# Kernel tuning notes

Hardware: AMD Instinct MI355X
Metric: run time of the kernel (lower is better)

## Reference

```python
import jax, jax.numpy as jnp
import numpy as np

B, D_IN, H, LAT = 4096, 4096, 4096, 512


def setup_inputs() -> dict:
    key = jax.random.key(0)
    ks = jax.random.split(key, 10)
    s = lambda fan_in: 1.0 / np.sqrt(fan_in)
    return {
        "x": jax.random.normal(ks[0], (B, D_IN), jnp.float32),
        "W_e1": jax.random.normal(ks[1], (D_IN, H), jnp.float32) * s(D_IN),
        "b_e1": jax.random.uniform(ks[2], (H,), jnp.float32),
        "W_e2": jax.random.normal(ks[3], (H, 2 * LAT), jnp.float32) * s(H),
        "b_e2": jax.random.uniform(ks[4], (2 * LAT,), jnp.float32),
        "W_d1": jax.random.normal(ks[5], (LAT, H), jnp.float32) * s(LAT),
        "b_d1": jax.random.uniform(ks[6], (H,), jnp.float32),
        "W_d2": jax.random.normal(ks[7], (H, D_IN), jnp.float32) * s(H),
        "b_d2": jax.random.uniform(ks[8], (D_IN,), jnp.float32),
        "eps": jax.random.normal(ks[9], (B, LAT), jnp.float32),
    }


def reference(x, W_e1, b_e1, W_e2, b_e2, W_d1, b_d1, W_d2, b_d2, eps):
    # encoder MLP
    h = jax.nn.relu(x @ W_e1 + b_e1)
    z = h @ W_e2 + b_e2                      # [B, 2*LAT]
    mu, logvar = z[:, :LAT], z[:, LAT:]
    # reparameterize: cholesky(diag(exp(logvar))) @ eps + mu == exp(0.5*logvar)*eps + mu
    zs = mu + jnp.exp(0.5 * logvar) * eps    # [B, LAT]
    # decoder MLP
    hd = jax.nn.relu(zs @ W_d1 + b_d1)
    recon = hd @ W_d2 + b_d2                 # [B, D_IN]
    return recon, mu, logvar
```

## Files before the change

### kernel.cpp

```cpp
#include <hip/hip_runtime.h>
#include <hip/hip_bf16.h>

typedef __attribute__((ext_vector_type(8))) __bf16 bf16x8;
typedef __attribute__((ext_vector_type(4))) float f32x4;
typedef __attribute__((ext_vector_type(4))) unsigned short ushort4v;
typedef unsigned short u16;

__device__ __forceinline__ u16 f2bf_bits(float f) {
    union { float f; unsigned int u; } x; x.f = f;
    unsigned int r = x.u + 0x7FFFu + ((x.u >> 16) & 1u);
    return (u16)(r >> 16);
}

__device__ __forceinline__ void gload_lds16(const void* g, void* l) {
    __builtin_amdgcn_global_load_lds(
        (const __attribute__((address_space(1))) void*)g,
        (__attribute__((address_space(3))) void*)l, 16, 0, 0);
}

#define BARRIER()  __builtin_amdgcn_s_barrier()
#define LGKM0()    asm volatile("s_waitcnt lgkmcnt(0)" ::: "memory")
#define VMW8()     asm volatile("s_waitcnt vmcnt(8)" ::: "memory")
#define VMW0()     asm volatile("s_waitcnt vmcnt(0)" ::: "memory")

__global__ void cvt4(const float* __restrict__ in, u16* __restrict__ out, int n) {
    int i = (blockIdx.x * 256 + threadIdx.x) << 2;
    if (i >= n) return;
    f32x4 v = *reinterpret_cast<const f32x4*>(in + i);
    ushort4v o;
    o.x = f2bf_bits(v.x); o.y = f2bf_bits(v.y);
    o.z = f2bf_bits(v.z); o.w = f2bf_bits(v.w);
    *reinterpret_cast<ushort4v*>(out + i) = o;
}

__global__ __launch_bounds__(256)
void transpose_cvt64(const float* __restrict__ in, u16* __restrict__ out,
                     int R, int C) {
    __shared__ float t[64][67];
    const int c0 = blockIdx.x << 6;
    const int r0 = blockIdx.y << 6;
    const int tx = threadIdx.x & 15;
    const int ty = threadIdx.x >> 4;
    #pragma unroll
    for (int j = 0; j < 4; ++j) {
        f32x4 v = *reinterpret_cast<const f32x4*>(
            &in[(size_t)(r0 + ty + 16 * j) * C + c0 + (tx << 2)]);
        *reinterpret_cast<f32x4*>(&t[ty + 16 * j][tx << 2]) = v;
    }
    __syncthreads();
    const int oc = threadIdx.x >> 2;
    const int rr = (threadIdx.x & 3) << 2;
    #pragma unroll
    for (int j = 0; j < 4; ++j) {
        const int r = rr + 16 * j;
        ushort4v o;
        o.x = f2bf_bits(t[r + 0][oc]);
        o.y = f2bf_bits(t[r + 1][oc]);
        o.z = f2bf_bits(t[r + 2][oc]);
        o.w = f2bf_bits(t[r + 3][oc]);
        *reinterpret_cast<ushort4v*>(&out[(size_t)(c0 + oc) * R + r0 + r]) = o;
    }
}

__global__ void sampler(const float* __restrict__ mu, const float* __restrict__ lv,
                        const float* __restrict__ eps, u16* __restrict__ zs, int n) {
    int i = blockIdx.x * 256 + threadIdx.x;
    if (i >= n) return;
    float v = mu[i] + __expf(0.5f * lv[i]) * eps[i];
    zs[i] = f2bf_bits(v);
}

template<int MODE>
__global__ __launch_bounds__(256)
void gemm_bt(const u16* __restrict__ A, const u16* __restrict__ Bt,
             const float* __restrict__ bias,
             u16* __restrict__ obf, float* __restrict__ of32, float* __restrict__ olv,
             int M, int N, int K)
{
    __shared__ u16 As[128 * 32];
    __shared__ u16 Bs[128 * 32];

    const int tid  = threadIdx.x;
    const int lane = tid & 63;
    const int w    = tid >> 6;
    const int wr   = w >> 1;
    const int wc   = w & 1;

    const int nbx  = N >> 7;
    const int brow = (blockIdx.x / nbx) << 7;
    const int bcol = (blockIdx.x % nbx) << 7;

    const int srow = (w << 4) + (lane >> 2);
    const int scol = (lane & 3) << 3;
    const size_t aoff0 = (size_t)(brow + srow) * K + scol;
    const size_t aoff1 = (size_t)(brow + 64 + srow) * K + scol;
    const size_t boff0 = (size_t)(bcol + srow) * K + scol;
    const size_t boff1 = (size_t)(bcol + 64 + srow) * K + scol;

    u16* asl0 = &As[(w << 9)];
    u16* asl1 = &As[2048 + (w << 9)];
    u16* bsl0 = &Bs[(w << 9)];
    u16* bsl1 = &Bs[2048 + (w << 9)];

    f32x4 acc[4][4];
    #pragma unroll
    for (int m = 0; m < 4; ++m)
        #pragma unroll
        for (int n = 0; n < 4; ++n)
            acc[m][n] = (f32x4)(0.0f);

    const int ar   = (wr << 6) + (lane & 15);
    const int br   = (wc << 6) + (lane & 15);
    const int koff = (lane >> 4) << 3;

    for (int kt = 0; kt < K; kt += 32) {
        __syncthreads();
        gload_lds16(A  + aoff0 + kt, asl0);
        gload_lds16(A  + aoff1 + kt, asl1);
        gload_lds16(Bt + boff0 + kt, bsl0);
        gload_lds16(Bt + boff1 + kt, bsl1);
        __syncthreads();

        bf16x8 av[4], bv[4];
        #pragma unroll
        for (int m = 0; m < 4; ++m)
            av[m] = *reinterpret_cast<const bf16x8*>(&As[(ar + (m << 4)) * 32 + koff]);
        #pragma unroll
        for (int n = 0; n < 4; ++n)
            bv[n] = *reinterpret_cast<const bf16x8*>(&Bs[(br + (n << 4)) * 32 + koff]);

        #pragma unroll
        for (int m = 0; m < 4; ++m)
            #pragma unroll
            for (int n = 0; n < 4; ++n)
                acc[m][n] = __builtin_amdgcn_mfma_f32_16x16x32_bf16(
                    av[m], bv[n], acc[m][n], 0, 0, 0);
    }

    float bv4[4];
    #pragma unroll
    for (int n = 0; n < 4; ++n)
        bv4[n] = bias[bcol + (wc << 6) + (n << 4) + (lane & 15)];

    const int erow0 = brow + (wr << 6) + ((lane >> 4) << 2);
    const int ecol0 = bcol + (wc << 6) + (lane & 15);

    #pragma unroll
    for (int m = 0; m < 4; ++m) {
        #pragma unroll
        for (int i = 0; i < 4; ++i) {
            const int r = erow0 + (m << 4) + i;
            #pragma unroll
            for (int n = 0; n < 4; ++n) {
                const int c = ecol0 + (n << 4);
                float v = acc[m][n][i] + bv4[n];
                if (MODE == 0) {
                    v = v > 0.0f ? v : 0.0f;
                    obf[(size_t)r * N + c] = f2bf_bits(v);
                } else if (MODE == 1) {
                    of32[(size_t)r * N + c] = v;
                } else {
                    if (c < 512) of32[(size_t)r * 512 + c] = v;
                    else         olv[(size_t)r * 512 + (c - 512)] = v;
                }
            }
        }
    }
}

template<int MODE>
__global__ __launch_bounds__(512, 2)
void gemm256(const u16* __restrict__ A, const u16* __restrict__ Bt,
             const float* __restrict__ bias,
             u16* __restrict__ obf, float* __restrict__ of32,
             int M, int N, int K)
{
    extern __shared__ char lds[];
    const int tid  = threadIdx.x;
    const int lane = tid & 63;
    const int w    = tid >> 6;
    const int wr   = w >> 2;
    const int wc   = w & 3;

    int bid = blockIdx.x;
    const int cpx = gridDim.x >> 3;
    bid = (bid & 7) * cpx + (bid >> 3);
    const int nbx  = N >> 8;
    const int brow = (bid / nbx) << 8;
    const int bcol = (bid % nbx) << 8;

    const int srow  = tid >> 3;
    const int scole = (((tid & 7) ^ (srow & 7)) << 4) >> 1;
    const size_t aoff = (size_t)(brow + srow) * K + scole;
    const size_t boff = (size_t)(bcol + srow) * K + scole;
    const size_t rowK64 = (size_t)64 * K;
    const int wave1024 = w << 10;

    const int lo16 = (lane >> 4) << 4;
    const int swzm = (lane & 7) << 4;
    const int low0 = lo16 ^ swzm;
    const int low1 = (64 | lo16) ^ swzm;
    const int rA   = (lane & 15) << 7;
    const int rB   = ((((wc & 1) << 6) | (lane & 15)) << 7);
    const int regA = wr << 14;
    const int regB = 32768 + ((wc >> 1) << 14);

    bf16x8 a[4][2];
    bf16x8 b0[2][2];
    bf16x8 b1[2][2];
    f32x4 acc[8][4];
    #pragma unroll
    for (int m = 0; m < 8; ++m)
        #pragma unroll
        for (int n = 0; n < 4; ++n)
            acc[m][n] = (f32x4)(0.0f);

#define STAGE_A(buf, h, kt) do { \
    const u16* _s = A + aoff + (size_t)(h) * 128 * K + (size_t)(kt) * 64; \
    gload_lds16(_s,          lds + ((buf) << 16) + ((h) << 14) + wave1024); \
    gload_lds16(_s + rowK64, lds + ((buf) << 16) + ((h) << 14) + 8192 + wave1024); \
} while (0)

#define STAGE_B(buf, h, kt) do { \
    const u16* _s = Bt + boff + (size_t)(h) * 128 * K + (size_t)(kt) * 64; \
    gload_lds16(_s,          lds + ((buf) << 16) + 32768 + ((h) << 14) + wave1024); \
    gload_lds16(_s + rowK64, lds + ((buf) << 16) + 32768 + ((h) << 14) + 8192 + wave1024); \
} while (0)

#define READ_A(buf, g) do { \
    _Pragma("unroll") \
    for (int m = 0; m < 4; ++m) { \
        const int _b = ((buf) << 16) + regA + rA + ((((g) << 2) + m) << 11); \
        a[m][0] = *reinterpret_cast<const bf16x8*>(lds + _b + low0); \
        a[m][1] = *reinterpret_cast<const bf16x8*>(lds + _b + low1); \
    } \
} while (0)

#define READ_B0(buf) do { \
    _Pragma("unroll") \
    for (int n = 0; n < 2; ++n) { \
        const int _b = ((buf) << 16) + regB + rB + (n << 11); \
        b0[n][0] = *reinterpret_cast<const bf16x8*>(lds + _b + low0); \
        b0[n][1] = *reinterpret_cast<const bf16x8*>(lds + _b + low1); \
    } \
} while (0)

#define READ_B1(buf) do { \
    _Pragma("unroll") \
    for (int n = 0; n < 2; ++n) { \
        const int _b = ((buf) << 16) + regB + rB + ((n + 2) << 11); \
        b1[n][0] = *reinterpret_cast<const bf16x8*>(lds + _b + low0); \
        b1[n][1] = *reinterpret_cast<const bf16x8*>(lds + _b + low1); \
    } \
} while (0)

#define MM(bx, mb, nb) do { \
    __builtin_amdgcn_s_setprio(1); \
    _Pragma("unroll") \
    for (int m = 0; m < 4; ++m) \
        _Pragma("unroll") \
        for (int n = 0; n < 2; ++n) \
            _Pragma("unroll") \
            for (int s = 0; s < 2; ++s) \
                acc[(mb) + m][(nb) + n] = __builtin_amdgcn_mfma_f32_16x16x32_bf16( \
                    a[m][s], bx[n][s], acc[(mb) + m][(nb) + n], 0, 0, 0); \
    __builtin_amdgcn_s_setprio(0); \
} while (0)

#define PH_SYNC() do { BARRIER(); LGKM0(); } while (0)
#define PH_END()  do { BARRIER(); } while (0)

    const int NT  = K >> 6;
    const int NIT = K >> 7;

    STAGE_A(0, 0, 0); STAGE_A(0, 1, 0); STAGE_B(0, 0, 0); STAGE_B(0, 1, 0);
    STAGE_A(1, 0, 1); STAGE_A(1, 1, 1); STAGE_B(1, 0, 1); STAGE_B(1, 1, 1);
    VMW8(); BARRIER();

    for (int it = 0; it < NIT; ++it) {
        const int tn0r = 2 * it + 2;
        const int tn1r = 2 * it + 3;
        const int tn0 = tn0r < NT ? tn0r : NT - 1;
        const int tn1 = tn1r < NT ? tn1r : NT - 1;

        READ_A(0, 0); READ_B0(0);
        PH_SYNC(); MM(b0, 0, 0); PH_END();

        READ_B1(0);
        STAGE_B(0, 0, tn0);
        PH_SYNC(); MM(b1, 0, 2); PH_END();

        READ_A(0, 1);
        STAGE_B(0, 1, tn0);
        PH_SYNC(); MM(b1, 4, 2); PH_END();

        STAGE_A(0, 0, tn0); STAGE_A(0, 1, tn0);
        PH_SYNC(); MM(b0, 4, 0);
        VMW8();
        BARRIER();

        READ_A(1, 0); READ_B0(1);
        PH_SYNC(); MM(b0, 0, 0); PH_END();

        READ_B1(1);
        STAGE_B(1, 0, tn1);
        PH_SYNC(); MM(b1, 0, 2); PH_END();

        READ_A(1, 1);
        STAGE_B(1, 1, tn1);
        PH_SYNC(); MM(b1, 4, 2); PH_END();

        STAGE_A(1, 0, tn1); STAGE_A(1, 1, tn1);
        PH_SYNC(); MM(b0, 4, 0);
        VMW8();
        BARRIER();
    }
    VMW0();

    float bb[4];
    #pragma unroll
    for (int n = 0; n < 4; ++n)
        bb[n] = bias[bcol + (wc << 6) + (n << 4) + (lane & 15)];

    const int erow0 = brow + (wr << 7) + ((lane >> 4) << 2);
    const int ecol0 = bcol + (wc << 6) + (lane & 15);

    #pragma unroll
    for (int m = 0; m < 8; ++m) {
        #pragma unroll
        for (int i = 0; i < 4; ++i) {
            const int r = erow0 + (m << 4) + i;
            #pragma unroll
            for (int n = 0; n < 4; ++n) {
                const int c = ecol0 + (n << 4);
                float v = acc[m][n][i] + bb[n];
                if (MODE == 0) {
                    v = v > 0.0f ? v : 0.0f;
                    obf[(size_t)r * N + c] = f2bf_bits(v);
                } else {
                    of32[(size_t)r * N + c] = v;
                }
            }
        }
    }
#undef STAGE_A
#undef STAGE_B
#undef READ_A
#undef READ_B0
#undef READ_B1
#undef MM
#undef PH_SYNC
#undef PH_END
}

extern "C" void kernel_launch(void* const* d_in, const int* in_sizes, int n_in,
                              void* d_out, int out_size, void* d_ws, size_t ws_size,
                              hipStream_t stream) {
    const float* x   = (const float*)d_in[0];
    const float* We1 = (const float*)d_in[1];
    const float* be1 = (const float*)d_in[2];
    const float* We2 = (const float*)d_in[3];
    const float* be2 = (const float*)d_in[4];
    const float* Wd1 = (const float*)d_in[5];
    const float* bd1 = (const float*)d_in[6];
    const float* Wd2 = (const float*)d_in[7];
    const float* bd2 = (const float*)d_in[8];
    const float* eps = (const float*)d_in[9];

    const int B = 4096, D = 4096, H = 4096, LAT = 512;

    char* ws = (char*)d_ws;
    u16* xb  = (u16*)(ws);
    u16* w1t = (u16*)(ws + 33554432);
    u16* w2t = (u16*)(ws + 67108864);
    u16* w3t = (u16*)(ws + 75497472);
    u16* w4t = (u16*)(ws + 79691776);
    u16* h   = (u16*)(ws + 113246208);
    u16* zs  = w1t;
    u16* hd  = xb;

    float* recon = (float*)d_out;
    float* mu    = recon + (size_t)B * D;
    float* lv    = mu + (size_t)B * LAT;

    hipFuncSetAttribute(reinterpret_cast<const void*>(gemm256<0>),
                        hipFuncAttributeMaxDynamicSharedMemorySize, 131072);
    hipFuncSetAttribute(reinterpret_cast<const void*>(gemm256<1>),
                        hipFuncAttributeMaxDynamicSharedMemorySize, 131072);

    cvt4<<<(B * D / 4 + 255) / 256, 256, 0, stream>>>(x, xb, B * D);
    transpose_cvt64<<<dim3(H / 64, D / 64), 256, 0, stream>>>(We1, w1t, D, H);
    transpose_cvt64<<<dim3(2 * LAT / 64, H / 64), 256, 0, stream>>>(We2, w2t, H, 2 * LAT);
    transpose_cvt64<<<dim3(H / 64, LAT / 64), 256, 0, stream>>>(Wd1, w3t, LAT, H);
    transpose_cvt64<<<dim3(D / 64, H / 64), 256, 0, stream>>>(Wd2, w4t, H, D);

    gemm256<0><<<(B / 256) * (H / 256), 512, 131072, stream>>>(xb, w1t, be1, h, nullptr, B, H, D);
    gemm_bt<2><<<(B / 128) * (2 * LAT / 128), 256, 0, stream>>>(h, w2t, be2, nullptr, mu, lv, B, 2 * LAT, H);
    sampler<<<(B * LAT + 255) / 256, 256, 0, stream>>>(mu, lv, eps, zs, B * LAT);
    gemm_bt<0><<<(B / 128) * (H / 128), 256, 0, stream>>>(zs, w3t, bd1, hd, nullptr, nullptr, B, H, LAT);
    gemm256<1><<<(B / 256) * (D / 256), 512, 131072, stream>>>(hd, w4t, bd2, nullptr, recon, B, D, H);
}
```

Measured before the change: 431.5 us.

## Software-pipeline LDS fragment reads under MFMA and use 256 tile GEMM for decoder layer one

The gemm256 main loop now issues the next phase's LDS fragment reads right after each MFMA block rather than before it, so shared-memory reads overlap the matrix math. The first fragments are preloaded before the loop, and the global-load wait is relaxed to vmcnt(4) at a different point. The decoder's first layer (K=512) also moves from the 128-tile gemm_bt kernel to the 256-tile gemm256 kernel. This adds reordering risk around barriers and waitcnts, the final vmcnt(0) drain after the loop is removed, and the larger tile gives fewer blocks for the short-K layer.

```diff
diff --git a/kernel.cpp b/kernel.cpp
--- a/kernel.cpp
+++ b/kernel.cpp
@@ -21,7 +21,7 @@
 #define BARRIER()  __builtin_amdgcn_s_barrier()
 #define LGKM0()    asm volatile("s_waitcnt lgkmcnt(0)" ::: "memory")
 #define VMW8()     asm volatile("s_waitcnt vmcnt(8)" ::: "memory")
-#define VMW0()     asm volatile("s_waitcnt vmcnt(0)" ::: "memory")
+#define VMW4()     asm volatile("s_waitcnt vmcnt(4)" ::: "memory")
 
 __global__ void cvt4(const float* __restrict__ in, u16* __restrict__ out, int n) {
     int i = (blockIdx.x * 256 + threadIdx.x) << 2;
@@ -267,15 +267,13 @@
     __builtin_amdgcn_s_setprio(0); \
 } while (0)
 
-#define PH_SYNC() do { BARRIER(); LGKM0(); } while (0)
-#define PH_END()  do { BARRIER(); } while (0)
-
     const int NT  = K >> 6;
     const int NIT = K >> 7;
 
     STAGE_A(0, 0, 0); STAGE_A(0, 1, 0); STAGE_B(0, 0, 0); STAGE_B(0, 1, 0);
     STAGE_A(1, 0, 1); STAGE_A(1, 1, 1); STAGE_B(1, 0, 1); STAGE_B(1, 1, 1);
     VMW8(); BARRIER();
+    READ_A(0, 0); READ_B0(0);
 
     for (int it = 0; it < NIT; ++it) {
         const int tn0r = 2 * it + 2;
@@ -283,39 +281,52 @@
         const int tn0 = tn0r < NT ? tn0r : NT - 1;
         const int tn1 = tn1r < NT ? tn1r : NT - 1;
 
+        BARRIER(); LGKM0();
+        MM(b0, 0, 0);
+        READ_B1(0);
+        BARRIER();
+        STAGE_B(0, 0, tn0);
+
+        BARRIER(); LGKM0();
+        MM(b1, 0, 2);
+        READ_A(0, 1);
+        BARRIER();
+        STAGE_B(0, 1, tn0);
+
+        BARRIER(); LGKM0();
+        MM(b1, 4, 2);
+        VMW4();
+        BARRIER();
+        STAGE_A(0, 0, tn0); STAGE_A(0, 1, tn0);
+
+        BARRIER(); LGKM0();
+        MM(b0, 4, 0);
+        READ_A(1, 0); READ_B0(1);
+        BARRIER();
+
+        BARRIER(); LGKM0();
+        MM(b0, 0, 0);
+        READ_B1(1);
+        BARRIER();
+        STAGE_B(1, 0, tn1);
+
+        BARRIER(); LGKM0();
+        MM(b1, 0, 2);
+        READ_A(1, 1);
+        BARRIER();
+        STAGE_B(1, 1, tn1);
+
+        BARRIER(); LGKM0();
+        MM(b1, 4, 2);
+        VMW4();
+        BARRIER();
+        STAGE_A(1, 0, tn1); STAGE_A(1, 1, tn1);
+
+        BARRIER(); LGKM0();
+        MM(b0, 4, 0);
         READ_A(0, 0); READ_B0(0);
-        PH_SYNC(); MM(b0, 0, 0); PH_END();
-
-        READ_B1(0);
-        STAGE_B(0, 0, tn0);
-        PH_SYNC(); MM(b1, 0, 2); PH_END();
-
-        READ_A(0, 1);
-        STAGE_B(0, 1, tn0);
-        PH_SYNC(); MM(b1, 4, 2); PH_END();
-
-        STAGE_A(0, 0, tn0); STAGE_A(0, 1, tn0);
-        PH_SYNC(); MM(b0, 4, 0);
-        VMW8();
-        BARRIER();
-
-        READ_A(1, 0); READ_B0(1);
-        PH_SYNC(); MM(b0, 0, 0); PH_END();
-
-        READ_B1(1);
-        STAGE_B(1, 0, tn1);
-        PH_SYNC(); MM(b1, 0, 2); PH_END();
-
-        READ_A(1, 1);
-        STAGE_B(1, 1, tn1);
-        PH_SYNC(); MM(b1, 4, 2); PH_END();
-
-        STAGE_A(1, 0, tn1); STAGE_A(1, 1, tn1);
-        PH_SYNC(); MM(b0, 4, 0);
-        VMW8();
-        BARRIER();
-    }
-    VMW0();
+        BARRIER();
+    }
 
     float bb[4];
     #pragma unroll
@@ -349,8 +360,6 @@
 #undef READ_B0
 #undef READ_B1
 #undef MM
-#undef PH_SYNC
-#undef PH_END
 }
 
 extern "C" void kernel_launch(void* const* d_in, const int* in_sizes, int n_in,
@@ -397,6 +406,6 @@
     gemm256<0><<<(B / 256) * (H / 256), 512, 131072, stream>>>(xb, w1t, be1, h, nullptr, B, H, D);
     gemm_bt<2><<<(B / 128) * (2 * LAT / 128), 256, 0, stream>>>(h, w2t, be2, nullptr, mu, lv, B, 2 * LAT, H);
     sampler<<<(B * LAT + 255) / 256, 256, 0, stream>>>(mu, lv, eps, zs, B * LAT);
-    gemm_bt<0><<<(B / 128) * (H / 128), 256, 0, stream>>>(zs, w3t, bd1, hd, nullptr, nullptr, B, H, LAT);
+    gemm256<0><<<(B / 256) * (H / 256), 512, 131072, stream>>>(zs, w3t, bd1, hd, nullptr, B, H, LAT);
     gemm256<1><<<(B / 256) * (D / 256), 512, 131072, stream>>>(hd, w4t, bd2, nullptr, recon, B, D, H);
 }
```

New measurement: 419.1 us. -2.9%, faster.
